# Performance work log

Hardware: AMD Instinct MI355X
Metric: run time of the kernel (lower is better)

The kernel has to match this reference:

```python
import jax, jax.numpy as jnp
import numpy as np

B, N, H = 8, 1024, 768
INNER = 64
ENT = 9
NEG = 1e12


def setup_inputs() -> dict:
    key = jax.random.key(0)
    ks = jax.random.split(key, 4)
    return {
        "last_hidden_state": jax.random.normal(ks[0], (B, N, H), dtype=jnp.float32),
        "attention_mask": jnp.ones((B, N), dtype=jnp.float32),
        "w1": jax.random.normal(ks[1], (H, 2 * INNER), dtype=jnp.float32) * 0.02,
        "b1": jnp.zeros((2 * INNER,), dtype=jnp.float32),
        "w2": jax.random.normal(ks[2], (H, 2 * ENT), dtype=jnp.float32) * 0.02,
        "b2": jnp.zeros((2 * ENT,), dtype=jnp.float32),
    }


def reference(last_hidden_state, attention_mask, w1, b1, w2, b2):
    b, n, _ = last_hidden_state.shape
    outputs = last_hidden_state @ w1 + b1            # (b, n, 2*inner)
    qw, kw = outputs[..., ::2], outputs[..., 1::2]   # (b, n, inner) each

    # Sinusoidal RoPE, 'zero' merge mode: even slots sin, odd slots cos
    half = INNER // 2
    inv_freq = jnp.power(10000.0, -2.0 * jnp.arange(half, dtype=jnp.float32) / INNER)
    ang = jnp.arange(n, dtype=jnp.float32)[:, None] * inv_freq[None, :]  # (n, half)
    sin_pos = jnp.repeat(jnp.sin(ang), 2, axis=-1)[None]  # (1, n, inner)
    cos_pos = jnp.repeat(jnp.cos(ang), 2, axis=-1)[None]

    def rope(x):
        # interleave (-x_odd, x_even)
        x2 = jnp.stack([-x[..., 1::2], x[..., ::2]], axis=-1).reshape(x.shape)
        return x * cos_pos + x2 * sin_pos

    qw, kw = rope(qw), rope(kw)

    logits = jnp.einsum('bmd,bnd->bmn', qw, kw) / jnp.sqrt(jnp.float32(INNER))
    bias = jnp.einsum('bnh->bhn', last_hidden_state @ w2 + b2) / 2.0  # (b, 2*ent, n)
    logits = logits[:, None] + bias[:, ::2, None] + bias[:, 1::2, :, None]  # (b,ent,n,n)

    # sequence masking on both trailing axes
    m = attention_mask.astype(logits.dtype)
    m_row = m[:, None, :, None]
    m_col = m[:, None, None, :]
    logits = logits * m_row + (-NEG) * (1.0 - m_row)
    logits = logits * m_col + (-NEG) * (1.0 - m_col)

    # strict lower-triangular suppression
    tril = jnp.tril(jnp.ones((n, n), dtype=logits.dtype), k=-1)
    logits = logits - tril * NEG
    return logits
```

## Files before the change

### kernel.cpp

```cpp
#include <hip/hip_runtime.h>
#include <cmath>

constexpr int kB = 8;
constexpr int kN = 1024;
constexpr int kH = 768;
constexpr float kNeg = 1000000000000.0f;

__global__ __launch_bounds__(512) void k1_proj_rope(
    const float* __restrict__ lhs, const float* __restrict__ w1,
    const float* __restrict__ b1, const float* __restrict__ w2,
    const float* __restrict__ b2, float* __restrict__ qw,
    float* __restrict__ kw, float* __restrict__ biasT)
{
  constexpr int CH = 96;
  constexpr int XP = 100;
  __shared__ float ws1[CH * 128];
  __shared__ float xs[32 * XP];

  const int t = threadIdx.x;
  const int g0 = blockIdx.x * 32;
  const int c = t & 31;
  const int rp = t >> 5;

  float acc0[4] = {0.f, 0.f, 0.f, 0.f};
  float acc1[4] = {0.f, 0.f, 0.f, 0.f};

  const int row0 = t / 18, col0 = t % 18;
  const int row1 = (t + 512) / 18, col1 = (t + 512) % 18;
  float sb0 = 0.f, sb1 = 0.f;

  for (int ch = 0; ch < 8; ++ch) {
    const float4* w1g = reinterpret_cast<const float4*>(w1 + (size_t)ch * CH * 128);
    float4* ws4 = reinterpret_cast<float4*>(ws1);
#pragma unroll
    for (int p = 0; p < 6; ++p) ws4[t + p * 512] = w1g[t + p * 512];
#pragma unroll
    for (int p = 0; p < 2; ++p) {
      const int idx = t + p * 512;
      if (idx < 768) {
        const int row = idx / 24, c4 = idx % 24;
        *reinterpret_cast<float4*>(&xs[row * XP + c4 * 4]) =
            *reinterpret_cast<const float4*>(
                &lhs[(size_t)(g0 + row) * kH + ch * CH + c4 * 4]);
      }
    }
    __syncthreads();

    const float* xr0 = &xs[rp * XP];
    const float* xr1 = &xs[(rp + 16) * XP];
    for (int h = 0; h < CH; h += 4) {
      float x0[4], x1[4];
      *reinterpret_cast<float4*>(x0) = *reinterpret_cast<const float4*>(&xr0[h]);
      *reinterpret_cast<float4*>(x1) = *reinterpret_cast<const float4*>(&xr1[h]);
#pragma unroll
      for (int hh = 0; hh < 4; ++hh) {
        const float4 wv = *reinterpret_cast<const float4*>(&ws1[(h + hh) * 128 + 4 * c]);
        acc0[0] += x0[hh] * wv.x; acc0[1] += x0[hh] * wv.y;
        acc0[2] += x0[hh] * wv.z; acc0[3] += x0[hh] * wv.w;
        acc1[0] += x1[hh] * wv.x; acc1[1] += x1[hh] * wv.y;
        acc1[2] += x1[hh] * wv.z; acc1[3] += x1[hh] * wv.w;
      }
    }

    {
      const int hb = ch * CH;
      const float* xr = &xs[row0 * XP];
      for (int h = 0; h < CH; h += 4) {
        const float4 xv = *reinterpret_cast<const float4*>(&xr[h]);
        sb0 += xv.x * w2[(size_t)(hb + h) * 18 + col0];
        sb0 += xv.y * w2[(size_t)(hb + h + 1) * 18 + col0];
        sb0 += xv.z * w2[(size_t)(hb + h + 2) * 18 + col0];
        sb0 += xv.w * w2[(size_t)(hb + h + 3) * 18 + col0];
      }
      if (t < 64) {
        const float* xr1b = &xs[row1 * XP];
        for (int h = 0; h < CH; h += 4) {
          const float4 xv = *reinterpret_cast<const float4*>(&xr1b[h]);
          sb1 += xv.x * w2[(size_t)(hb + h) * 18 + col1];
          sb1 += xv.y * w2[(size_t)(hb + h + 1) * 18 + col1];
          sb1 += xv.z * w2[(size_t)(hb + h + 2) * 18 + col1];
          sb1 += xv.w * w2[(size_t)(hb + h + 3) * 18 + col1];
        }
      }
    }
    __syncthreads();
  }

  float bb[4];
  *reinterpret_cast<float4*>(bb) = *reinterpret_cast<const float4*>(&b1[4 * c]);
  const float inv = exp2f(-(float)c * 0.41524101186092f);
#pragma unroll
  for (int rr = 0; rr < 2; ++rr) {
    const float* acc = rr ? acc1 : acc0;
    const int g = g0 + rp + rr * 16;
    const int n = g & (kN - 1);
    float si, co;
    sincosf((float)n * inv, &si, &co);
    const float oq0 = acc[0] + bb[0], ok0 = acc[1] + bb[1];
    const float oq1 = acc[2] + bb[2], ok1 = acc[3] + bb[3];
    float2 qv = make_float2(oq0 * co - oq1 * si, oq1 * co + oq0 * si);
    float2 kv = make_float2(ok0 * co - ok1 * si, ok1 * co + ok0 * si);
    *reinterpret_cast<float2*>(&qw[(size_t)g * 64 + 2 * c]) = qv;
    *reinterpret_cast<float2*>(&kw[(size_t)g * 64 + 2 * c]) = kv;
  }

  {
    const int g = g0 + row0;
    const int b = g >> 10, n = g & (kN - 1);
    biasT[((size_t)b * 18 + col0) * kN + n] = (sb0 + b2[col0]) * 0.5f;
  }
  if (t < 64) {
    const int g = g0 + row1;
    const int b = g >> 10, n = g & (kN - 1);
    biasT[((size_t)b * 18 + col1) * kN + n] = (sb1 + b2[col1]) * 0.5f;
  }
}

__global__ __launch_bounds__(256) void k2_logits(
    const float* __restrict__ qw, const float* __restrict__ kw,
    const float* __restrict__ biasT, const float* __restrict__ mask,
    float* __restrict__ out)
{
  constexpr int LD = 68;
  __shared__ float smem[64 * LD * 2 + 576 * 2 + 128];
  float* qs = smem;
  float* ks = smem + 64 * LD;
  float* ts = smem;
  float* bE = smem + 128 * LD;
  float* bO = bE + 576;
  float* mr_s = bO + 576;
  float* mc_s = mr_s + 64;

  const int t = threadIdx.x;
  const int b = blockIdx.z;
  const int m0 = blockIdx.y * 64;
  const int n0 = blockIdx.x * 64;

  const float* qg = qw + ((size_t)b * kN + m0) * 64;
  const float* kg = kw + ((size_t)b * kN + n0) * 64;
#pragma unroll
  for (int p = 0; p < 4; ++p) {
    const int idx = t + p * 256;
    const int row = idx >> 4;
    const int c4 = (idx & 15) << 2;
    *reinterpret_cast<float4*>(&qs[row * LD + c4]) =
        *reinterpret_cast<const float4*>(&qg[row * 64 + c4]);
    *reinterpret_cast<float4*>(&ks[row * LD + c4]) =
        *reinterpret_cast<const float4*>(&kg[row * 64 + c4]);
  }
  for (int idx = t; idx < 576; idx += 256) {
    const int e = idx >> 6, x = idx & 63;
    bE[idx] = biasT[((size_t)b * 18 + 2 * e) * kN + n0 + x];
    bO[idx] = biasT[((size_t)b * 18 + 2 * e + 1) * kN + m0 + x];
  }
  if (t < 64) mr_s[t] = mask[b * kN + m0 + t];
  else if (t < 128) mc_s[t - 64] = mask[b * kN + n0 + (t - 64)];
  __syncthreads();

  const int tx = t & 15;
  const int ty = t >> 4;
  const int ml = ty << 2;

  float acc[4][4] = {};
  for (int d = 0; d < 64; d += 4) {
    float4 q[4], k[4];
#pragma unroll
    for (int i = 0; i < 4; ++i)
      q[i] = *reinterpret_cast<const float4*>(&qs[(ml + i) * LD + d]);
#pragma unroll
    for (int j = 0; j < 4; ++j)
      k[j] = *reinterpret_cast<const float4*>(&ks[(tx + 16 * j) * LD + d]);
#pragma unroll
    for (int i = 0; i < 4; ++i)
#pragma unroll
      for (int j = 0; j < 4; ++j)
        acc[i][j] += q[i].x * k[j].x + q[i].y * k[j].y +
                     q[i].z * k[j].z + q[i].w * k[j].w;
  }

  __syncthreads();
#pragma unroll
  for (int i = 0; i < 4; ++i)
#pragma unroll
    for (int j = 0; j < 4; ++j)
      ts[(ml + i) * LD + tx + 16 * j] = acc[i][j] * 0.125f;
  __syncthreads();

  const int rb = ml;
  const int cb = tx << 2;
  float4 sv[4];
#pragma unroll
  for (int i = 0; i < 4; ++i)
    sv[i] = *reinterpret_cast<const float4*>(&ts[(rb + i) * LD + cb]);

  const float4 mrv = *reinterpret_cast<const float4*>(&mr_s[rb]);
  const float4 mcv = *reinterpret_cast<const float4*>(&mc_s[cb]);
  const float mrA[4] = {mrv.x, mrv.y, mrv.z, mrv.w};
  const float mcA[4] = {mcv.x, mcv.y, mcv.z, mcv.w};

  const size_t obase =
      (size_t)b * 9 * kN * kN + (size_t)(m0 + rb) * kN + (n0 + cb);
  for (int e = 0; e < 9; ++e) {
    const float4 bev = *reinterpret_cast<const float4*>(&bE[e * 64 + cb]);
    const float4 bov = *reinterpret_cast<const float4*>(&bO[e * 64 + rb]);
    const float beA[4] = {bev.x, bev.y, bev.z, bev.w};
    const float boA[4] = {bov.x, bov.y, bov.z, bov.w};
    float* oe = out + obase + (size_t)e * kN * kN;
#pragma unroll
    for (int i = 0; i < 4; ++i) {
      const int m = m0 + rb + i;
      const float* s = reinterpret_cast<const float*>(&sv[i]);
      float4 v4;
      float* v = reinterpret_cast<float*>(&v4);
#pragma unroll
      for (int cc = 0; cc < 4; ++cc) {
        const int n = n0 + cb + cc;
        float val = s[cc] + beA[cc] + boA[i];
        val = val * mrA[i] - kNeg * (1.f - mrA[i]);
        val = val * mcA[cc] - kNeg * (1.f - mcA[cc]);
        if (m > n) val -= kNeg;
        v[cc] = val;
      }
      *reinterpret_cast<float4*>(&oe[(size_t)i * kN]) = v4;
    }
  }
}

extern "C" void kernel_launch(void* const* d_in, const int* in_sizes, int n_in,
                              void* d_out, int out_size, void* d_ws, size_t ws_size,
                              hipStream_t stream) {
  const float* lhs  = (const float*)d_in[0];
  const float* mask = (const float*)d_in[1];
  const float* w1   = (const float*)d_in[2];
  const float* b1   = (const float*)d_in[3];
  const float* w2   = (const float*)d_in[4];
  const float* b2   = (const float*)d_in[5];
  float* out = (float*)d_out;

  float* qw    = (float*)d_ws;
  float* kwp   = qw  + (size_t)kB * kN * 64;
  float* biasT = kwp + (size_t)kB * kN * 64;

  k1_proj_rope<<<dim3(kB * kN / 32), 512, 0, stream>>>(lhs, w1, b1, w2, b2,
                                                       qw, kwp, biasT);
  k2_logits<<<dim3(kN / 64, kN / 64, kB), 256, 0, stream>>>(qw, kwp, biasT,
                                                            mask, out);
}
```

Measured before the change: 426.8 us.

## Store RoPE'd q/k as bf16 and compute logits tile with MFMA

The projection kernel now writes q and k in bf16 instead of fp32, and the logits kernel computes each 64x64 tile with bf16 MFMA 16x16x32 instructions fed directly from global memory. This drops the shared-memory staging and the scalar FMA dot-product loop. The epilogue now stores scalar floats laid out per the MFMA fragment (16 consecutive columns per row) rather than float4 rows, and bias and mask values are read straight from global memory. The output write of 302 MB dominates the runtime, so the gain is bounded, and bf16 adds rounding error to the logits.

```diff
diff --git a/kernel.cpp b/kernel.cpp
--- a/kernel.cpp
+++ b/kernel.cpp
@@ -1,4 +1,5 @@
 #include <hip/hip_runtime.h>
+#include <hip/hip_bf16.h>
 #include <cmath>
 
 constexpr int kB = 8;
@@ -6,11 +7,14 @@
 constexpr int kH = 768;
 constexpr float kNeg = 1000000000000.0f;
 
+typedef __attribute__((ext_vector_type(8))) short s8v;
+typedef __attribute__((ext_vector_type(4))) float f4v;
+
 __global__ __launch_bounds__(512) void k1_proj_rope(
     const float* __restrict__ lhs, const float* __restrict__ w1,
     const float* __restrict__ b1, const float* __restrict__ w2,
-    const float* __restrict__ b2, float* __restrict__ qw,
-    float* __restrict__ kw, float* __restrict__ biasT)
+    const float* __restrict__ b2, __hip_bfloat16* __restrict__ qw,
+    __hip_bfloat16* __restrict__ kw, float* __restrict__ biasT)
 {
   constexpr int CH = 96;
   constexpr int XP = 100;
@@ -98,10 +102,13 @@
     sincosf((float)n * inv, &si, &co);
     const float oq0 = acc[0] + bb[0], ok0 = acc[1] + bb[1];
     const float oq1 = acc[2] + bb[2], ok1 = acc[3] + bb[3];
-    float2 qv = make_float2(oq0 * co - oq1 * si, oq1 * co + oq0 * si);
-    float2 kv = make_float2(ok0 * co - ok1 * si, ok1 * co + ok0 * si);
-    *reinterpret_cast<float2*>(&qw[(size_t)g * 64 + 2 * c]) = qv;
-    *reinterpret_cast<float2*>(&kw[(size_t)g * 64 + 2 * c]) = kv;
+    __hip_bfloat162 qv, kv;
+    qv.x = __float2bfloat16(oq0 * co - oq1 * si);
+    qv.y = __float2bfloat16(oq1 * co + oq0 * si);
+    kv.x = __float2bfloat16(ok0 * co - ok1 * si);
+    kv.y = __float2bfloat16(ok1 * co + ok0 * si);
+    *reinterpret_cast<__hip_bfloat162*>(&qw[(size_t)g * 64 + 2 * c]) = qv;
+    *reinterpret_cast<__hip_bfloat162*>(&kw[(size_t)g * 64 + 2 * c]) = kv;
   }
 
   {
@@ -117,111 +124,69 @@
 }
 
 __global__ __launch_bounds__(256) void k2_logits(
-    const float* __restrict__ qw, const float* __restrict__ kw,
+    const __hip_bfloat16* __restrict__ qw, const __hip_bfloat16* __restrict__ kw,
     const float* __restrict__ biasT, const float* __restrict__ mask,
     float* __restrict__ out)
 {
-  constexpr int LD = 68;
-  __shared__ float smem[64 * LD * 2 + 576 * 2 + 128];
-  float* qs = smem;
-  float* ks = smem + 64 * LD;
-  float* ts = smem;
-  float* bE = smem + 128 * LD;
-  float* bO = bE + 576;
-  float* mr_s = bO + 576;
-  float* mc_s = mr_s + 64;
-
   const int t = threadIdx.x;
+  const int lane = t & 63;
+  const int wid = t >> 6;
+  const int tx = lane & 15;
+  const int quad = lane >> 4;
   const int b = blockIdx.z;
   const int m0 = blockIdx.y * 64;
   const int n0 = blockIdx.x * 64;
-
-  const float* qg = qw + ((size_t)b * kN + m0) * 64;
-  const float* kg = kw + ((size_t)b * kN + n0) * 64;
-#pragma unroll
-  for (int p = 0; p < 4; ++p) {
-    const int idx = t + p * 256;
-    const int row = idx >> 4;
-    const int c4 = (idx & 15) << 2;
-    *reinterpret_cast<float4*>(&qs[row * LD + c4]) =
-        *reinterpret_cast<const float4*>(&qg[row * 64 + c4]);
-    *reinterpret_cast<float4*>(&ks[row * LD + c4]) =
-        *reinterpret_cast<const float4*>(&kg[row * 64 + c4]);
-  }
-  for (int idx = t; idx < 576; idx += 256) {
-    const int e = idx >> 6, x = idx & 63;
-    bE[idx] = biasT[((size_t)b * 18 + 2 * e) * kN + n0 + x];
-    bO[idx] = biasT[((size_t)b * 18 + 2 * e + 1) * kN + m0 + x];
-  }
-  if (t < 64) mr_s[t] = mask[b * kN + m0 + t];
-  else if (t < 128) mc_s[t - 64] = mask[b * kN + n0 + (t - 64)];
-  __syncthreads();
-
-  const int tx = t & 15;
-  const int ty = t >> 4;
-  const int ml = ty << 2;
-
-  float acc[4][4] = {};
-  for (int d = 0; d < 64; d += 4) {
-    float4 q[4], k[4];
-#pragma unroll
-    for (int i = 0; i < 4; ++i)
-      q[i] = *reinterpret_cast<const float4*>(&qs[(ml + i) * LD + d]);
-#pragma unroll
-    for (int j = 0; j < 4; ++j)
-      k[j] = *reinterpret_cast<const float4*>(&ks[(tx + 16 * j) * LD + d]);
-#pragma unroll
-    for (int i = 0; i < 4; ++i)
-#pragma unroll
-      for (int j = 0; j < 4; ++j)
-        acc[i][j] += q[i].x * k[j].x + q[i].y * k[j].y +
-                     q[i].z * k[j].z + q[i].w * k[j].w;
-  }
-
-  __syncthreads();
-#pragma unroll
-  for (int i = 0; i < 4; ++i)
-#pragma unroll
-    for (int j = 0; j < 4; ++j)
-      ts[(ml + i) * LD + tx + 16 * j] = acc[i][j] * 0.125f;
-  __syncthreads();
-
-  const int rb = ml;
-  const int cb = tx << 2;
-  float4 sv[4];
-#pragma unroll
-  for (int i = 0; i < 4; ++i)
-    sv[i] = *reinterpret_cast<const float4*>(&ts[(rb + i) * LD + cb]);
-
-  const float4 mrv = *reinterpret_cast<const float4*>(&mr_s[rb]);
-  const float4 mcv = *reinterpret_cast<const float4*>(&mc_s[cb]);
-  const float mrA[4] = {mrv.x, mrv.y, mrv.z, mrv.w};
-  const float mcA[4] = {mcv.x, mcv.y, mcv.z, mcv.w};
-
-  const size_t obase =
-      (size_t)b * 9 * kN * kN + (size_t)(m0 + rb) * kN + (n0 + cb);
+  const int ms = m0 + wid * 16;
+
+  const short* qp =
+      reinterpret_cast<const short*>(qw) + ((size_t)b * kN + ms + tx) * 64;
+  const short* kp =
+      reinterpret_cast<const short*>(kw) + ((size_t)b * kN + n0 + tx) * 64;
+
+  const s8v a0 = *reinterpret_cast<const s8v*>(qp + quad * 8);
+  const s8v a1 = *reinterpret_cast<const s8v*>(qp + 32 + quad * 8);
+
+  f4v acc[4] = {f4v{0,0,0,0}, f4v{0,0,0,0}, f4v{0,0,0,0}, f4v{0,0,0,0}};
+#pragma unroll
+  for (int j = 0; j < 4; ++j) {
+    const short* kj = kp + (size_t)j * 16 * 64;
+    const s8v b0 = *reinterpret_cast<const s8v*>(kj + quad * 8);
+    const s8v b1 = *reinterpret_cast<const s8v*>(kj + 32 + quad * 8);
+    acc[j] = __builtin_amdgcn_mfma_f32_16x16x32_bf16(a0, b0, acc[j], 0, 0, 0);
+    acc[j] = __builtin_amdgcn_mfma_f32_16x16x32_bf16(a1, b1, acc[j], 0, 0, 0);
+  }
+
+  const float* mrow = mask + (size_t)b * kN;
+  float mc[4], mr[4];
+#pragma unroll
+  for (int j = 0; j < 4; ++j) mc[j] = mrow[n0 + 16 * j + tx];
+#pragma unroll
+  for (int r = 0; r < 4; ++r) mr[r] = mrow[ms + quad * 4 + r];
+
+  const size_t obb = (size_t)b * 9 * kN * kN;
   for (int e = 0; e < 9; ++e) {
-    const float4 bev = *reinterpret_cast<const float4*>(&bE[e * 64 + cb]);
-    const float4 bov = *reinterpret_cast<const float4*>(&bO[e * 64 + rb]);
-    const float beA[4] = {bev.x, bev.y, bev.z, bev.w};
-    const float boA[4] = {bov.x, bov.y, bov.z, bov.w};
-    float* oe = out + obase + (size_t)e * kN * kN;
-#pragma unroll
-    for (int i = 0; i < 4; ++i) {
-      const int m = m0 + rb + i;
-      const float* s = reinterpret_cast<const float*>(&sv[i]);
-      float4 v4;
-      float* v = reinterpret_cast<float*>(&v4);
-#pragma unroll
-      for (int cc = 0; cc < 4; ++cc) {
-        const int n = n0 + cb + cc;
-        float val = s[cc] + beA[cc] + boA[i];
-        val = val * mrA[i] - kNeg * (1.f - mrA[i]);
-        val = val * mcA[cc] - kNeg * (1.f - mcA[cc]);
-        if (m > n) val -= kNeg;
-        v[cc] = val;
-      }
-      *reinterpret_cast<float4*>(&oe[(size_t)i * kN]) = v4;
+    const float* bEr = biasT + ((size_t)b * 18 + 2 * e) * kN;
+    const float* bOr = biasT + ((size_t)b * 18 + 2 * e + 1) * kN;
+    float be[4], bo[4];
+#pragma unroll
+    for (int j = 0; j < 4; ++j) be[j] = bEr[n0 + 16 * j + tx];
+#pragma unroll
+    for (int r = 0; r < 4; ++r) bo[r] = bOr[ms + quad * 4 + r];
+
+    float* oe = out + obb + (size_t)e * kN * kN;
+#pragma unroll
+    for (int r = 0; r < 4; ++r) {
+      const int m = ms + quad * 4 + r;
+      float* orow = oe + (size_t)m * kN;
+#pragma unroll
+      for (int j = 0; j < 4; ++j) {
+        const int n = n0 + 16 * j + tx;
+        float v = acc[j][r] * 0.125f + be[j] + bo[r];
+        v = v * mr[r] - kNeg * (1.f - mr[r]);
+        v = v * mc[j] - kNeg * (1.f - mc[j]);
+        if (m > n) v -= kNeg;
+        orow[n] = v;
+      }
     }
   }
 }
@@ -237,9 +202,9 @@
   const float* b2   = (const float*)d_in[5];
   float* out = (float*)d_out;
 
-  float* qw    = (float*)d_ws;
-  float* kwp   = qw  + (size_t)kB * kN * 64;
-  float* biasT = kwp + (size_t)kB * kN * 64;
+  __hip_bfloat16* qw  = (__hip_bfloat16*)d_ws;
+  __hip_bfloat16* kwp = qw + (size_t)kB * kN * 64;
+  float* biasT = (float*)(kwp + (size_t)kB * kN * 64);
 
   k1_proj_rope<<<dim3(kB * kN / 32), 512, 0, stream>>>(lhs, w1, b1, w2, b2,
                                                        qw, kwp, biasT);
```

Result: no change. 425.8 us (-0.2%).
